# Kernel optimization log

Hardware: AMD Instinct MI355X
Metric: run time of the kernel (lower is better)

Reference implementation:

```python
import jax, jax.numpy as jnp
import numpy as np

EPS = 1e-5

def conv1x1(x, w, b):
    # x: [B,C,H,W], w: [O,C], b: [O]
    return jnp.einsum('bchw,oc->bohw', x, w) + b[None, :, None, None]

def bn_eval(x, w, b, m, v):
    inv = w / jnp.sqrt(v + EPS)
    return (x - m[None, :, None, None]) * inv[None, :, None, None] + b[None, :, None, None]

def setup_inputs() -> dict:
    key = jax.random.key(0)
    ks = jax.random.split(key, 32)
    B, Fg, Fl, Fi, H, W = 4, 128, 128, 64, 64, 64
    d = {}
    d['g'] = jax.random.normal(ks[0], (B, Fg, H, W), jnp.float32)
    d['x'] = jax.random.normal(ks[1], (B, Fl, H, W), jnp.float32)
    d['wg_w'] = jax.random.normal(ks[2], (Fi, Fg), jnp.float32) * 0.1
    d['wg_b'] = jax.random.normal(ks[3], (Fi,), jnp.float32) * 0.1
    d['bng_w'] = jax.random.uniform(ks[4], (Fi,), jnp.float32)
    d['bng_b'] = jax.random.normal(ks[5], (Fi,), jnp.float32) * 0.1
    d['bng_m'] = jax.random.normal(ks[6], (Fi,), jnp.float32) * 0.1
    d['bng_v'] = jax.random.uniform(ks[7], (Fi,), jnp.float32) + 0.5
    d['wx_w'] = jax.random.normal(ks[8], (Fi, Fl), jnp.float32) * 0.1
    d['wx_b'] = jax.random.normal(ks[9], (Fi,), jnp.float32) * 0.1
    d['bnx_w'] = jax.random.uniform(ks[10], (Fi,), jnp.float32)
    d['bnx_b'] = jax.random.normal(ks[11], (Fi,), jnp.float32) * 0.1
    d['bnx_m'] = jax.random.normal(ks[12], (Fi,), jnp.float32) * 0.1
    d['bnx_v'] = jax.random.uniform(ks[13], (Fi,), jnp.float32) + 0.5
    d['q_w'] = jax.random.normal(ks[14], (Fi // 8, Fi), jnp.float32) * 0.1
    d['q_b'] = jax.random.normal(ks[15], (Fi // 8,), jnp.float32) * 0.1
    d['k_w'] = jax.random.normal(ks[16], (Fi // 8, Fi), jnp.float32) * 0.1
    d['k_b'] = jax.random.normal(ks[17], (Fi // 8,), jnp.float32) * 0.1
    d['v_w'] = jax.random.normal(ks[18], (Fi, Fi), jnp.float32) * 0.1
    d['v_b'] = jax.random.normal(ks[19], (Fi,), jnp.float32) * 0.1
    d['sa_gamma'] = jax.random.normal(ks[20], (1,), jnp.float32)
    d['psi_w'] = jax.random.normal(ks[21], (1, Fi), jnp.float32) * 0.1
    d['psi_b'] = jax.random.normal(ks[22], (1,), jnp.float32) * 0.1
    d['bnp_w'] = jax.random.uniform(ks[23], (1,), jnp.float32)
    d['bnp_b'] = jax.random.normal(ks[24], (1,), jnp.float32) * 0.1
    d['bnp_m'] = jax.random.normal(ks[25], (1,), jnp.float32) * 0.1
    d['bnp_v'] = jax.random.uniform(ks[26], (1,), jnp.float32) + 0.5
    return d

def reference(g, x, wg_w, wg_b, bng_w, bng_b, bng_m, bng_v,
              wx_w, wx_b, bnx_w, bnx_b, bnx_m, bnx_v,
              q_w, q_b, k_w, k_b, v_w, v_b, sa_gamma,
              psi_w, psi_b, bnp_w, bnp_b, bnp_m, bnp_v):
    g1 = bn_eval(conv1x1(g, wg_w, wg_b), bng_w, bng_b, bng_m, bng_v)
    x1 = bn_eval(conv1x1(x, wx_w, wx_b), bnx_w, bnx_b, bnx_m, bnx_v)
    c = jax.nn.relu(g1 + x1)  # [B, Fi, H, W]
    B, C, H, W = c.shape
    N = H * W
    q = conv1x1(c, q_w, q_b).reshape(B, -1, N)  # [B, Fi/8, N]
    k = conv1x1(c, k_w, k_b).reshape(B, -1, N)
    v = conv1x1(c, v_w, v_b).reshape(B, C, N)
    energy = jnp.einsum('bcn,bcm->bnm', q, k)    # [B, N, N]
    attn = jax.nn.softmax(energy, axis=-1)
    sa_out = jnp.einsum('bcm,bnm->bcn', v, attn).reshape(B, C, H, W)
    attended = sa_gamma[0] * sa_out + c
    psi = jax.nn.sigmoid(bn_eval(conv1x1(attended, psi_w, psi_b), bnp_w, bnp_b, bnp_m, bnp_v))
    return x * psi
```

## Files before the change

kernel.cpp:

```cpp
#include <hip/hip_runtime.h>
#include <hip/hip_bf16.h>


typedef short bf16x8 __attribute__((ext_vector_type(8)));
typedef unsigned short u16x8 __attribute__((ext_vector_type(8)));
typedef unsigned short u16x4 __attribute__((ext_vector_type(4)));
typedef float f32x4 __attribute__((ext_vector_type(4)));

__device__ __forceinline__ unsigned short f2b16(float f) {
  return __builtin_bit_cast(unsigned short, __float2bfloat16(f));
}
__device__ __forceinline__ float b2f(unsigned short u) {
  return __bfloat162float(__builtin_bit_cast(__hip_bfloat16, u));
}

#define EPSV 1e-5f
#define LOG2E 1.44269504088896340736f

#define C_OFF      0u
#define Q_OFF      (C_OFF + 2097152u)
#define K_OFF      (Q_OFF + 262144u)
#define V_OFF      (K_OFF + 262144u)
#define OPART_OFF  (V_OFF + 2097152u)
#define ML_OFF     (OPART_OFF + 16777216u)

__global__ __launch_bounds__(256) void conv_fused_kernel(
    const float* __restrict__ g, const float* __restrict__ x,
    const float* __restrict__ wg_w, const float* __restrict__ wg_b,
    const float* __restrict__ bng_w, const float* __restrict__ bng_b,
    const float* __restrict__ bng_m, const float* __restrict__ bng_v,
    const float* __restrict__ wx_w, const float* __restrict__ wx_b,
    const float* __restrict__ bnx_w, const float* __restrict__ bnx_b,
    const float* __restrict__ bnx_m, const float* __restrict__ bnx_v,
    const float* __restrict__ q_w, const float* __restrict__ q_b,
    const float* __restrict__ k_w, const float* __restrict__ k_b,
    const float* __restrict__ v_w, const float* __restrict__ v_b,
    unsigned short* __restrict__ cb, unsigned short* __restrict__ Qb,
    unsigned short* __restrict__ Kb, unsigned short* __restrict__ Vb)
{
  __shared__ __attribute__((aligned(16))) unsigned short xt[16][264];
  __shared__ __attribute__((aligned(16))) unsigned short clds[16][72];
  __shared__ __attribute__((aligned(16))) unsigned short vstage[64][20];

  const int t = threadIdx.x;
  const int bid = blockIdx.x;
  const int b = bid >> 8;
  const int n0 = (bid & 255) << 4;

  {
    const int col4 = t & 3;
    const int rowg = t >> 2;
    float4 v[4];
    #pragma unroll
    for (int rr = 0; rr < 4; ++rr) {
      int row = rowg * 4 + rr;
      const float* src = (row < 128)
          ? (g + ((size_t)(b * 128 + row)) * 4096 + n0 + col4 * 4)
          : (x + ((size_t)(b * 128 + (row - 128))) * 4096 + n0 + col4 * 4);
      v[rr] = *(const float4*)src;
    }
    #pragma unroll
    for (int j = 0; j < 4; ++j) {
      u16x4 pk;
      #pragma unroll
      for (int rr = 0; rr < 4; ++rr)
        pk[rr] = f2b16(((const float*)&v[rr])[j]);
      *(u16x4*)(&xt[col4 * 4 + j][rowg * 4]) = pk;
    }
  }

  const int l = t & 63, w = t >> 6;
  const int l15 = l & 15, lg = l >> 4;
  f32x4 zf = {0.f, 0.f, 0.f, 0.f};

  const int orow = w * 16 + l15;
  const float invg = bng_w[orow] * rsqrtf(bng_v[orow] + EPSV);
  const float invx = bnx_w[orow] * rsqrtf(bnx_v[orow] + EPSV);
  bf16x8 afrag[8];
  #pragma unroll
  for (int ks = 0; ks < 8; ++ks) {
    int k = ks * 32 + lg * 8;
    const float* wp;
    float sc;
    if (k < 128) { wp = wg_w + orow * 128 + k;         sc = invg; }
    else         { wp = wx_w + orow * 128 + (k - 128); sc = invx; }
    float4 w0 = *(const float4*)wp;
    float4 w1 = *(const float4*)(wp + 4);
    u16x8 pk;
    pk[0] = f2b16(w0.x * sc); pk[1] = f2b16(w0.y * sc);
    pk[2] = f2b16(w0.z * sc); pk[3] = f2b16(w0.w * sc);
    pk[4] = f2b16(w1.x * sc); pk[5] = f2b16(w1.y * sc);
    pk[6] = f2b16(w1.z * sc); pk[7] = f2b16(w1.w * sc);
    afrag[ks] = __builtin_bit_cast(bf16x8, pk);
  }
  __syncthreads();

  f32x4 acc = zf;
  #pragma unroll
  for (int ks = 0; ks < 8; ++ks) {
    bf16x8 bfv = *(const bf16x8*)(&xt[l15][ks * 32 + lg * 8]);
    acc = __builtin_amdgcn_mfma_f32_16x16x32_bf16(afrag[ks], bfv, acc, 0, 0, 0);
  }
  #pragma unroll
  for (int r = 0; r < 4; ++r) {
    int o = w * 16 + lg * 4 + r;
    float ig = bng_w[o] * rsqrtf(bng_v[o] + EPSV);
    float ix = bnx_w[o] * rsqrtf(bnx_v[o] + EPSV);
    float bc = (wg_b[o] - bng_m[o]) * ig + bng_b[o]
             + (wx_b[o] - bnx_m[o]) * ix + bnx_b[o];
    float cv = fmaxf(acc[r] + bc, 0.f);
    unsigned short cv16 = f2b16(cv);
    cb[((size_t)(b * 64 + o)) * 4096 + n0 + l15] = cv16;
    clds[l15][o] = cv16;
  }
  __syncthreads();

  const int ngl = n0 + l15;
  #pragma unroll
  for (int i = 0; i < 2; ++i) {
    int t5 = w + 4 * i;
    if (t5 >= 5) break;
    int wrow = t5 * 16 + l15;
    f32x4 a2 = zf;
    #pragma unroll
    for (int kk = 0; kk < 2; ++kk) {
      int k = kk * 32 + lg * 8;
      const float* wp = (wrow < 8)  ? (q_w + wrow * 64 + k)
                      : (wrow < 16) ? (k_w + (wrow - 8) * 64 + k)
                                    : (v_w + (wrow - 16) * 64 + k);
      float4 w0 = *(const float4*)wp;
      float4 w1 = *(const float4*)(wp + 4);
      u16x8 pk;
      pk[0] = f2b16(w0.x); pk[1] = f2b16(w0.y);
      pk[2] = f2b16(w0.z); pk[3] = f2b16(w0.w);
      pk[4] = f2b16(w1.x); pk[5] = f2b16(w1.y);
      pk[6] = f2b16(w1.z); pk[7] = f2b16(w1.w);
      bf16x8 bfv = *(const bf16x8*)(&clds[l15][k]);
      a2 = __builtin_amdgcn_mfma_f32_16x16x32_bf16(
          __builtin_bit_cast(bf16x8, pk), bfv, a2, 0, 0, 0);
    }
    if (t5 == 0) {
      u16x4 pk;
      #pragma unroll
      for (int r = 0; r < 4; ++r) {
        int row = lg * 4 + r;
        float val;
        if (row < 8) val = (a2[r] + q_b[row]) * LOG2E;
        else         val = a2[r] + k_b[row - 8];
        pk[r] = f2b16(val);
      }
      if (lg < 2)
        *(u16x4*)(Qb + (((size_t)b << 12) + ngl) * 8 + lg * 4) = pk;
      else
        *(u16x4*)(Kb + (((size_t)b << 12) + ngl) * 8 + (lg - 2) * 4) = pk;
    } else {
      #pragma unroll
      for (int r = 0; r < 4; ++r) {
        int vch = (t5 - 1) * 16 + lg * 4 + r;
        vstage[vch][l15] = f2b16(a2[r] + v_b[vch]);
      }
    }
  }
  __syncthreads();

  {
    int row = t >> 2, seg = t & 3;
    u16x4 pv = *(const u16x4*)(&vstage[row][seg * 4]);
    *(u16x4*)(Vb + ((size_t)(b * 64 + row)) * 4096 + n0 + seg * 4) = pv;
  }
}

__global__ __launch_bounds__(256) void attn_partial_kernel(
    const unsigned short* __restrict__ Qb, const unsigned short* __restrict__ Kb,
    const unsigned short* __restrict__ Vb,
    unsigned short* __restrict__ Opart, float* __restrict__ ml)
{
  __shared__ __attribute__((aligned(16))) unsigned short klds[64][8];
  __shared__ __attribute__((aligned(16))) unsigned short vlds[64][72];
  __shared__ __attribute__((aligned(16))) unsigned short plds[4][16][72];

  const int t = threadIdx.x;
  const int bid = blockIdx.x;
  const int qt = bid & 63;
  const int b = (bid >> 6) & 3;
  const int ci = bid >> 8;
  const int n0 = qt << 6;
  const int l = t & 63, w = t >> 6;
  const int l15 = l & 15, lg = l >> 4;

  bf16x8 qf = {0, 0, 0, 0, 0, 0, 0, 0};
  if (lg == 0)
    qf = *(const bf16x8*)(Qb + (((size_t)b << 12) + n0 + w * 16 + l15) * 8);

  f32x4 zf = {0.f, 0.f, 0.f, 0.f};
  f32x4 O[4];
  O[0] = O[1] = O[2] = O[3] = zf;
  float m_run[4] = {-INFINITY, -INFINITY, -INFINITY, -INFINITY};
  float l_run[4] = {0.f, 0.f, 0.f, 0.f};

  const int m_lo = ci << 9, m_hi = (ci + 1) << 9;
  for (int m0 = m_lo; m0 < m_hi; m0 += 64) {
    if (t < 64)
      *(int4*)(&klds[t][0]) = *(const int4*)(Kb + (((size_t)b << 12) + m0 + t) * 8);
    #pragma unroll
    for (int i = 0; i < 2; ++i) {
      int ci2 = t + 256 * i;
      int row = ci2 >> 3, off = ci2 & 7;
      *(int4*)(&vlds[row][off * 8]) =
          *(const int4*)(Vb + ((size_t)(b * 64 + row)) * 4096 + m0 + off * 8);
    }
    __syncthreads();

    f32x4 e[4];
    #pragma unroll
    for (int mt = 0; mt < 4; ++mt) {
      bf16x8 kf = *(const bf16x8*)(&klds[mt * 16 + l15][0]);
      e[mt] = __builtin_amdgcn_mfma_f32_16x16x32_bf16(qf, kf, zf, 0, 0, 0);
    }

    #pragma unroll
    for (int r = 0; r < 4; ++r) {
      float vm = fmaxf(fmaxf(e[0][r], e[1][r]), fmaxf(e[2][r], e[3][r]));
      vm = fmaxf(vm, __shfl_xor(vm, 1));
      vm = fmaxf(vm, __shfl_xor(vm, 2));
      vm = fmaxf(vm, __shfl_xor(vm, 4));
      vm = fmaxf(vm, __shfl_xor(vm, 8));
      bool nosk = !__all(vm <= m_run[r] + 8.f);
      float nm = nosk ? fmaxf(m_run[r], vm) : m_run[r];
      float s = 0.f;
      #pragma unroll
      for (int mt = 0; mt < 4; ++mt) {
        float p = __builtin_amdgcn_exp2f(e[mt][r] - nm);
        e[mt][r] = p;
        s += p;
      }
      s += __shfl_xor(s, 1);
      s += __shfl_xor(s, 2);
      s += __shfl_xor(s, 4);
      s += __shfl_xor(s, 8);
      if (nosk) {
        float sc = __builtin_amdgcn_exp2f(m_run[r] - nm);
        l_run[r] = l_run[r] * sc + s;
        m_run[r] = nm;
        #pragma unroll
        for (int ct = 0; ct < 4; ++ct) O[ct][r] *= sc;
      } else {
        l_run[r] += s;
      }
      #pragma unroll
      for (int mt = 0; mt < 4; ++mt)
        plds[w][lg * 4 + r][mt * 16 + l15] = f2b16(e[mt][r]);
    }

    #pragma unroll
    for (int ct = 0; ct < 4; ++ct) {
      #pragma unroll
      for (int kk = 0; kk < 2; ++kk) {
        bf16x8 pa = *(const bf16x8*)(&plds[w][l15][kk * 32 + lg * 8]);
        bf16x8 vb = *(const bf16x8*)(&vlds[ct * 16 + l15][kk * 32 + lg * 8]);
        O[ct] = __builtin_amdgcn_mfma_f32_16x16x32_bf16(pa, vb, O[ct], 0, 0, 0);
      }
    }
    __syncthreads();
  }

  const size_t pb = ((size_t)(ci * 4 + b)) << 12;
  #pragma unroll
  for (int ct = 0; ct < 4; ++ct) {
    int ch = ct * 16 + l15;
    #pragma unroll
    for (int r = 0; r < 4; ++r) {
      int qg = n0 + w * 16 + lg * 4 + r;
      Opart[(pb + qg) * 64 + ch] = f2b16(O[ct][r]);
    }
  }
  if (l15 == 0) {
    #pragma unroll
    for (int r = 0; r < 4; ++r) {
      int qg = n0 + w * 16 + lg * 4 + r;
      float2 mv;
      mv.x = m_run[r]; mv.y = l_run[r];
      *(float2*)(ml + (pb + qg) * 2) = mv;
    }
  }
}

__global__ __launch_bounds__(256) void combine_kernel(
    const unsigned short* __restrict__ Opart, const float* __restrict__ ml,
    const unsigned short* __restrict__ cb, const float* __restrict__ xin,
    const float* __restrict__ psi_w, const float* __restrict__ psi_b,
    const float* __restrict__ bnp_w, const float* __restrict__ bnp_b,
    const float* __restrict__ bnp_m, const float* __restrict__ bnp_v,
    const float* __restrict__ sa_gamma,
    float* __restrict__ out)
{
  __shared__ __attribute__((aligned(16))) unsigned short c_lds[64][20];
  __shared__ __attribute__((aligned(8))) float2 ml_lds[16][8];
  __shared__ float psi_lds[16];

  const int t = threadIdx.x;
  const int bid = blockIdx.x;
  const int b = bid >> 8;
  const int n0 = (bid & 255) << 4;

  {
    int row = t >> 2, seg = t & 3;
    *(u16x4*)(&c_lds[row][seg * 4]) =
        *(const u16x4*)(cb + ((size_t)(b * 64 + row)) * 4096 + n0 + seg * 4);
  }
  if (t < 128) {
    int q = t >> 3, ci = t & 7;
    ml_lds[q][ci] = *(const float2*)(ml + ((((size_t)(ci * 4 + b)) << 12) + n0 + q) * 2);
  }
  __syncthreads();

  const float invp = bnp_w[0] * rsqrtf(bnp_v[0] + EPSV);
  const float psi_c = (psi_b[0] - bnp_m[0]) * invp + bnp_b[0];
  const float gamma = sa_gamma[0];

  const int q = t >> 4, cg = t & 15;
  const int qg = n0 + q;

  float M = -INFINITY;
  #pragma unroll
  for (int ci = 0; ci < 8; ++ci) M = fmaxf(M, ml_lds[q][ci].x);
  float L = 0.f, wgt[8];
  #pragma unroll
  for (int ci = 0; ci < 8; ++ci) {
    wgt[ci] = __builtin_amdgcn_exp2f(ml_lds[q][ci].x - M);
    L += wgt[ci] * ml_lds[q][ci].y;
  }
  float o4[4] = {0.f, 0.f, 0.f, 0.f};
  #pragma unroll
  for (int ci = 0; ci < 8; ++ci) {
    u16x4 p = *(const u16x4*)(Opart + ((((size_t)(ci * 4 + b)) << 12) + qg) * 64 + cg * 4);
    float wv = wgt[ci];
    #pragma unroll
    for (int k = 0; k < 4; ++k) o4[k] += wv * b2f(p[k]);
  }
  const float invL = 1.f / L;
  float ps = 0.f;
  #pragma unroll
  for (int k = 0; k < 4; ++k) {
    int ch = cg * 4 + k;
    ps += (psi_w[ch] * invp) * (gamma * (o4[k] * invL) + b2f(c_lds[ch][q]));
  }
  ps += __shfl_xor(ps, 1);
  ps += __shfl_xor(ps, 2);
  ps += __shfl_xor(ps, 4);
  ps += __shfl_xor(ps, 8);
  if (cg == 0)
    psi_lds[q] = 1.f / (1.f + __expf(-(ps + psi_c)));
  __syncthreads();

  #pragma unroll
  for (int i = 0; i < 2; ++i) {
    int idx = t + 256 * i;
    int f = idx >> 2, c4 = idx & 3;
    size_t off = ((size_t)(b * 128 + f)) * 4096 + n0 + c4 * 4;
    float4 xv = *(const float4*)(xin + off);
    float4 ov;
    ov.x = xv.x * psi_lds[c4 * 4 + 0];
    ov.y = xv.y * psi_lds[c4 * 4 + 1];
    ov.z = xv.z * psi_lds[c4 * 4 + 2];
    ov.w = xv.w * psi_lds[c4 * 4 + 3];
    *(float4*)(out + off) = ov;
  }
}

extern "C" void kernel_launch(void* const* d_in, const int* in_sizes, int n_in,
                              void* d_out, int out_size, void* d_ws, size_t ws_size,
                              hipStream_t stream) {
  (void)in_sizes; (void)n_in; (void)out_size; (void)ws_size;
  const float* g     = (const float*)d_in[0];
  const float* x     = (const float*)d_in[1];
  const float* wg_w  = (const float*)d_in[2];
  const float* wg_b  = (const float*)d_in[3];
  const float* bng_w = (const float*)d_in[4];
  const float* bng_b = (const float*)d_in[5];
  const float* bng_m = (const float*)d_in[6];
  const float* bng_v = (const float*)d_in[7];
  const float* wx_w  = (const float*)d_in[8];
  const float* wx_b  = (const float*)d_in[9];
  const float* bnx_w = (const float*)d_in[10];
  const float* bnx_b = (const float*)d_in[11];
  const float* bnx_m = (const float*)d_in[12];
  const float* bnx_v = (const float*)d_in[13];
  const float* q_w   = (const float*)d_in[14];
  const float* q_b   = (const float*)d_in[15];
  const float* k_w   = (const float*)d_in[16];
  const float* k_b   = (const float*)d_in[17];
  const float* v_w   = (const float*)d_in[18];
  const float* v_b   = (const float*)d_in[19];
  const float* sa_g  = (const float*)d_in[20];
  const float* psi_w = (const float*)d_in[21];
  const float* psi_b = (const float*)d_in[22];
  const float* bnp_w = (const float*)d_in[23];
  const float* bnp_b = (const float*)d_in[24];
  const float* bnp_m = (const float*)d_in[25];
  const float* bnp_v = (const float*)d_in[26];
  float* out = (float*)d_out;

  char* ws = (char*)d_ws;
  unsigned short* cb = (unsigned short*)(ws + C_OFF);
  unsigned short* Qb = (unsigned short*)(ws + Q_OFF);
  unsigned short* Kb = (unsigned short*)(ws + K_OFF);
  unsigned short* Vb = (unsigned short*)(ws + V_OFF);
  unsigned short* Opart = (unsigned short*)(ws + OPART_OFF);
  float* mlb = (float*)(ws + ML_OFF);

  hipLaunchKernelGGL(conv_fused_kernel, dim3(1024), dim3(256), 0, stream,
                     g, x, wg_w, wg_b, bng_w, bng_b, bng_m, bng_v,
                     wx_w, wx_b, bnx_w, bnx_b, bnx_m, bnx_v,
                     q_w, q_b, k_w, k_b, v_w, v_b,
                     cb, Qb, Kb, Vb);

  hipLaunchKernelGGL(attn_partial_kernel, dim3(2048), dim3(256), 0, stream,
                     Qb, Kb, Vb, Opart, mlb);

  hipLaunchKernelGGL(combine_kernel, dim3(1024), dim3(256), 0, stream,
                     Opart, mlb, cb, x,
                     psi_w, psi_b, bnp_w, bnp_b, bnp_m, bnp_v, sa_g,
                     out);
}
```

Measured before the change: 193.5 us.

## Transpose attention MFMAs so each lane owns one query row

Swaps the MFMA operand order in both the QK^T and PV products, so the energy and output accumulators are transposed and each lane holds a single query row. Row max and sum then need only two cross-lane shuffles instead of four per row, with one running max/sum per lane instead of four. P is written to LDS as packed 4-element vectors in a new [2][16][40] layout, and Opart stores become vectorized 4-wide writes. The cost is a more intricate P-layout index mapping that must exactly match the MFMA B-operand fragment layout.

```diff
diff --git a/kernel.cpp b/kernel.cpp
--- a/kernel.cpp
+++ b/kernel.cpp
@@ -177,7 +177,7 @@
 {
   __shared__ __attribute__((aligned(16))) unsigned short klds[64][8];
   __shared__ __attribute__((aligned(16))) unsigned short vlds[64][72];
-  __shared__ __attribute__((aligned(16))) unsigned short plds[4][16][72];
+  __shared__ __attribute__((aligned(16))) unsigned short plds[4][2][16][40];
 
   const int t = threadIdx.x;
   const int bid = blockIdx.x;
@@ -195,8 +195,8 @@
   f32x4 zf = {0.f, 0.f, 0.f, 0.f};
   f32x4 O[4];
   O[0] = O[1] = O[2] = O[3] = zf;
-  float m_run[4] = {-INFINITY, -INFINITY, -INFINITY, -INFINITY};
-  float l_run[4] = {0.f, 0.f, 0.f, 0.f};
+  float m_run = -INFINITY;
+  float l_run = 0.f;
 
   const int m_lo = ci << 9, m_hi = (ci + 1) << 9;
   for (int m0 = m_lo; m0 < m_hi; m0 += 64) {
@@ -215,73 +215,79 @@
     #pragma unroll
     for (int mt = 0; mt < 4; ++mt) {
       bf16x8 kf = *(const bf16x8*)(&klds[mt * 16 + l15][0]);
-      e[mt] = __builtin_amdgcn_mfma_f32_16x16x32_bf16(qf, kf, zf, 0, 0, 0);
-    }
-
-    #pragma unroll
-    for (int r = 0; r < 4; ++r) {
-      float vm = fmaxf(fmaxf(e[0][r], e[1][r]), fmaxf(e[2][r], e[3][r]));
-      vm = fmaxf(vm, __shfl_xor(vm, 1));
-      vm = fmaxf(vm, __shfl_xor(vm, 2));
-      vm = fmaxf(vm, __shfl_xor(vm, 4));
-      vm = fmaxf(vm, __shfl_xor(vm, 8));
-      bool nosk = !__all(vm <= m_run[r] + 8.f);
-      float nm = nosk ? fmaxf(m_run[r], vm) : m_run[r];
-      float s = 0.f;
-      #pragma unroll
-      for (int mt = 0; mt < 4; ++mt) {
+      e[mt] = __builtin_amdgcn_mfma_f32_16x16x32_bf16(kf, qf, zf, 0, 0, 0);
+    }
+
+    float vm = fmaxf(fmaxf(fmaxf(e[0][0], e[0][1]), fmaxf(e[0][2], e[0][3])),
+                     fmaxf(fmaxf(e[1][0], e[1][1]), fmaxf(e[1][2], e[1][3])));
+    float vm2 = fmaxf(fmaxf(fmaxf(e[2][0], e[2][1]), fmaxf(e[2][2], e[2][3])),
+                      fmaxf(fmaxf(e[3][0], e[3][1]), fmaxf(e[3][2], e[3][3])));
+    vm = fmaxf(vm, vm2);
+    vm = fmaxf(vm, __shfl_xor(vm, 16));
+    vm = fmaxf(vm, __shfl_xor(vm, 32));
+
+    bool nosk = __any(vm > m_run + 8.f);
+    float nm = nosk ? fmaxf(m_run, vm) : m_run;
+    float s = 0.f;
+    #pragma unroll
+    for (int mt = 0; mt < 4; ++mt) {
+      #pragma unroll
+      for (int r = 0; r < 4; ++r) {
         float p = __builtin_amdgcn_exp2f(e[mt][r] - nm);
         e[mt][r] = p;
         s += p;
       }
-      s += __shfl_xor(s, 1);
-      s += __shfl_xor(s, 2);
-      s += __shfl_xor(s, 4);
-      s += __shfl_xor(s, 8);
-      if (nosk) {
-        float sc = __builtin_amdgcn_exp2f(m_run[r] - nm);
-        l_run[r] = l_run[r] * sc + s;
-        m_run[r] = nm;
+    }
+    s += __shfl_xor(s, 16);
+    s += __shfl_xor(s, 32);
+    if (nosk) {
+      float sc = __builtin_amdgcn_exp2f(m_run - nm);
+      l_run = l_run * sc + s;
+      m_run = nm;
+      #pragma unroll
+      for (int ct = 0; ct < 4; ++ct)
         #pragma unroll
-        for (int ct = 0; ct < 4; ++ct) O[ct][r] *= sc;
-      } else {
-        l_run[r] += s;
+        for (int r = 0; r < 4; ++r) O[ct][r] *= sc;
+    } else {
+      l_run += s;
+    }
+
+    #pragma unroll
+    for (int mt = 0; mt < 4; ++mt) {
+      u16x4 pk;
+      #pragma unroll
+      for (int r = 0; r < 4; ++r) pk[r] = f2b16(e[mt][r]);
+      int kk = mt >> 1;
+      int lgr = 2 * (mt & 1) + (lg >> 1);
+      int j0 = 4 * (lg & 1);
+      *(u16x4*)(&plds[w][kk][l15][lgr * 8 + j0]) = pk;
+    }
+
+    #pragma unroll
+    for (int ct = 0; ct < 4; ++ct) {
+      #pragma unroll
+      for (int kk = 0; kk < 2; ++kk) {
+        bf16x8 pfr = *(const bf16x8*)(&plds[w][kk][l15][lg * 8]);
+        bf16x8 vf = *(const bf16x8*)(&vlds[ct * 16 + l15][kk * 32 + lg * 8]);
+        O[ct] = __builtin_amdgcn_mfma_f32_16x16x32_bf16(vf, pfr, O[ct], 0, 0, 0);
       }
-      #pragma unroll
-      for (int mt = 0; mt < 4; ++mt)
-        plds[w][lg * 4 + r][mt * 16 + l15] = f2b16(e[mt][r]);
-    }
-
-    #pragma unroll
-    for (int ct = 0; ct < 4; ++ct) {
-      #pragma unroll
-      for (int kk = 0; kk < 2; ++kk) {
-        bf16x8 pa = *(const bf16x8*)(&plds[w][l15][kk * 32 + lg * 8]);
-        bf16x8 vb = *(const bf16x8*)(&vlds[ct * 16 + l15][kk * 32 + lg * 8]);
-        O[ct] = __builtin_amdgcn_mfma_f32_16x16x32_bf16(pa, vb, O[ct], 0, 0, 0);
-      }
     }
     __syncthreads();
   }
 
   const size_t pb = ((size_t)(ci * 4 + b)) << 12;
+  const int qg = n0 + w * 16 + l15;
   #pragma unroll
   for (int ct = 0; ct < 4; ++ct) {
-    int ch = ct * 16 + l15;
-    #pragma unroll
-    for (int r = 0; r < 4; ++r) {
-      int qg = n0 + w * 16 + lg * 4 + r;
-      Opart[(pb + qg) * 64 + ch] = f2b16(O[ct][r]);
-    }
-  }
-  if (l15 == 0) {
-    #pragma unroll
-    for (int r = 0; r < 4; ++r) {
-      int qg = n0 + w * 16 + lg * 4 + r;
-      float2 mv;
-      mv.x = m_run[r]; mv.y = l_run[r];
-      *(float2*)(ml + (pb + qg) * 2) = mv;
-    }
+    u16x4 pk;
+    #pragma unroll
+    for (int r = 0; r < 4; ++r) pk[r] = f2b16(O[ct][r]);
+    *(u16x4*)(Opart + (pb + qg) * 64 + ct * 16 + lg * 4) = pk;
+  }
+  if (lg == 0) {
+    float2 mv;
+    mv.x = m_run; mv.y = l_run;
+    *(float2*)(ml + (pb + qg) * 2) = mv;
   }
 }
 
```

Result: faster. 172.9 us (-10.7%).
